# Optimization experiments

Hardware: AMD Instinct MI355X
Metric: run time of the kernel (lower is better)

The kernel has to match this reference:

```python
import jax, jax.numpy as jnp
import numpy as np

B, HF, WF = 16, 32, 32
DIM, NH = 1024, 16
HD = DIM // NH  # 64


def axial_freqs(H, W, head_dim):
    # RotaryEmbedding(dim=head_dim//4, freqs_for='pixel', max_freq=H*W)
    d = head_dim // 4  # rotary dim per axis
    base = jnp.linspace(1.0, (H * W) / 2.0, d // 2) * jnp.pi  # [d//2]
    posH = jnp.linspace(-1.0, 1.0, H)
    posW = jnp.linspace(-1.0, 1.0, W)
    fH = jnp.repeat(posH[:, None] * base[None, :], 2, axis=-1)  # [H, d]
    fW = jnp.repeat(posW[:, None] * base[None, :], 2, axis=-1)  # [W, d]
    fH = jnp.broadcast_to(fH[:, None, :], (H, W, d))
    fW = jnp.broadcast_to(fW[None, :, :], (H, W, d))
    return jnp.concatenate([fH, fW], axis=-1)  # [H, W, 2d] = [H, W, head_dim//2]


def rotate_half(x):
    # interleaved pair rotation: (x1, x2) -> (-x2, x1)
    xr = x.reshape(*x.shape[:-1], -1, 2)
    x1, x2 = xr[..., 0], xr[..., 1]
    return jnp.stack([-x2, x1], axis=-1).reshape(x.shape)


def apply_rotary(freqs, t):
    # t: [B, h, H, W, hd]; freqs: [H, W, rot_dim]
    rd = freqs.shape[-1]
    t_rot, t_pass = t[..., :rd], t[..., rd:]
    t_rot = t_rot * jnp.cos(freqs) + rotate_half(t_rot) * jnp.sin(freqs)
    return jnp.concatenate([t_rot, t_pass], axis=-1)


def setup_inputs() -> dict:
    key = jax.random.key(0)
    k1, k2, k3 = jax.random.split(key, 3)
    s = 1.0 / np.sqrt(DIM)
    return {
        "x": jax.random.normal(k1, (B, HF * WF, DIM), jnp.float32),
        "w_qkv": jax.random.normal(k2, (3 * DIM, DIM), jnp.float32) * s,
        "w_proj": jax.random.normal(k3, (DIM, DIM), jnp.float32) * s,
        "b_proj": jnp.zeros((DIM,), jnp.float32),
    }


def reference(x, w_qkv, w_proj, b_proj):
    freqs = axial_freqs(HF, WF, HD)
    qkv = x @ w_qkv.T  # [B, N, 3*DIM]
    q, k, v = jnp.split(qkv, 3, axis=-1)

    def to_grid(t):  # [B, N, DIM] -> [B, h, H, W, hd]
        return t.reshape(B, HF, WF, NH, HD).transpose(0, 3, 1, 2, 4)

    q, k, v = to_grid(q), to_grid(k), to_grid(v)
    q = apply_rotary(freqs, q)
    k = apply_rotary(freqs, k)
    N = HF * WF
    q = q.reshape(B, NH, N, HD)
    k = k.reshape(B, NH, N, HD)
    v = v.reshape(B, NH, N, HD)

    scale = 1.0 / np.sqrt(HD)
    attn = jax.nn.softmax(jnp.einsum('bhnd,bhmd->bhnm', q, k) * scale, axis=-1)
    out = jnp.einsum('bhnm,bhmd->bhnd', attn, v)  # [B, h, N, hd]
    out = out.transpose(0, 2, 1, 3).reshape(B, N, DIM)
    return out @ w_proj.T + b_proj
```

## Files before the change

### kernel.cpp

```cpp
#include <hip/hip_runtime.h>
#include <hip/hip_bf16.h>
#include <math.h>

typedef __bf16 bf16;
typedef bf16 bf16x4 __attribute__((ext_vector_type(4)));
typedef bf16 bf16x8 __attribute__((ext_vector_type(8)));
typedef float f32x4 __attribute__((ext_vector_type(4)));

#define MFMA16(a, b, c) __builtin_amdgcn_mfma_f32_16x16x32_bf16((a), (b), (c), 0, 0, 0)

#define QSCALE 0.18033688011112042f

__device__ __forceinline__ void async16(const void* g, void* l) {
  __builtin_amdgcn_global_load_lds(
      (const __attribute__((address_space(1))) void*)g,
      (__attribute__((address_space(3))) void*)l, 16, 0, 0);
}

__global__ __launch_bounds__(256) void f2b_kernel(const float* __restrict__ in,
                                                  bf16* __restrict__ out, int n) {
  int i = (blockIdx.x * 256 + threadIdx.x) * 4;
  if (i >= n) return;
  f32x4 v = *(const f32x4*)(in + i);
  bf16x4 o = {(bf16)v[0], (bf16)v[1], (bf16)v[2], (bf16)v[3]};
  *(bf16x4*)(out + i) = o;
}

__global__ __launch_bounds__(256) void table_kernel(float* __restrict__ cosT,
                                                    float* __restrict__ sinT) {
  int idx = blockIdx.x * 256 + threadIdx.x;
  if (idx >= 1024 * 32) return;
  int n = idx >> 5, d = idx & 31;
  int hf = n >> 5, wf = n & 31;
  int bi = (d & 15) >> 1;
  float base = (1.0f + 73.0f * bi) * 3.14159265358979323846f;
  int p = (d < 16) ? hf : wf;
  float pos = (2.0f * (float)p - 31.0f) * (1.0f / 31.0f);
  float f = pos * base;
  cosT[idx] = cosf(f);
  sinT[idx] = sinf(f);
}

template <int EPI, int NBN>
__global__ __launch_bounds__(512, 2) void gemm_bt(
    const bf16* __restrict__ A, const bf16* __restrict__ W,
    bf16* __restrict__ oq, bf16* __restrict__ okk, bf16* __restrict__ ovt,
    const float* __restrict__ cosT, const float* __restrict__ sinT,
    float* __restrict__ outF, const float* __restrict__ bias) {
  constexpr int K = 1024;
  __shared__ bf16 As[4][256 * 32];
  __shared__ bf16 Bs[4][256 * 32];

  const int tid = threadIdx.x;
  const int lane = tid & 63;
  const int wid = tid >> 6;
  const int lo = lane & 15, hi = lane >> 4;
  const int wm = wid >> 2;
  const int wn = wid & 3;

  const int wg = blockIdx.x;
  const int xcd = wg & 7;
  const int i = wg >> 3;
  const int bm = xcd * 8 + i / NBN;
  const int bn = i % NBN;

  const bf16* Ab = A + (size_t)bm * 256 * K;
  const bf16* Wb = W + (size_t)bn * 256 * K;

  const f32x4 fzero = {0.f, 0.f, 0.f, 0.f};
  f32x4 acc[8][4];
#pragma unroll
  for (int i2 = 0; i2 < 8; ++i2)
#pragma unroll
    for (int j = 0; j < 4; ++j) acc[i2][j] = fzero;

  size_t srcOff[2];
  int ldsOff[2];
#pragma unroll
  for (int i2 = 0; i2 < 2; ++i2) {
    const int c = i2 * 512 + tid;
    const int row = c >> 2, g = c & 3;
    const int gsrc = g ^ ((row >> 1) & 3);
    srcOff[i2] = (size_t)row * K + gsrc * 8;
    ldsOff[i2] = c * 8;
  }

  auto stageSlot = [&](int slot, int kh) {
#pragma unroll
    for (int i2 = 0; i2 < 2; ++i2)
      async16(Ab + srcOff[i2] + kh * 32, &As[slot][ldsOff[i2]]);
#pragma unroll
    for (int i2 = 0; i2 < 2; ++i2)
      async16(Wb + srcOff[i2] + kh * 32, &Bs[slot][ldsOff[i2]]);
  };

  auto compute = [&](int slot) {
    bf16x8 af[8], bf[4];
#pragma unroll
    for (int mf = 0; mf < 8; ++mf) {
      const int row = wm * 128 + mf * 16 + lo;
      const int g = hi ^ ((row >> 1) & 3);
      af[mf] = *(const bf16x8*)&As[slot][row * 32 + g * 8];
    }
#pragma unroll
    for (int nf = 0; nf < 4; ++nf) {
      const int row = wn * 64 + nf * 16 + lo;
      const int g = hi ^ ((row >> 1) & 3);
      bf[nf] = *(const bf16x8*)&Bs[slot][row * 32 + g * 8];
    }
    __builtin_amdgcn_s_setprio(1);
#pragma unroll
    for (int mf = 0; mf < 8; ++mf)
#pragma unroll
      for (int nf = 0; nf < 4; ++nf)
        acc[mf][nf] = MFMA16(af[mf], bf[nf], acc[mf][nf]);
    __builtin_amdgcn_s_setprio(0);
  };

  stageSlot(0, 0);
  stageSlot(1, 1);

  for (int kt = 0; kt < 7; ++kt) {
#pragma unroll
    for (int ph = 0; ph < 4; ++ph) {
      stageSlot((ph + 2) & 3, kt * 4 + ph + 2);
      asm volatile("s_waitcnt vmcnt(8)" ::: "memory");
      __builtin_amdgcn_s_barrier();
      compute(ph);
    }
  }
  stageSlot(2, 30);
  asm volatile("s_waitcnt vmcnt(8)" ::: "memory");
  __builtin_amdgcn_s_barrier();
  compute(0);
  stageSlot(3, 31);
  asm volatile("s_waitcnt vmcnt(8)" ::: "memory");
  __builtin_amdgcn_s_barrier();
  compute(1);
  asm volatile("s_waitcnt vmcnt(4)" ::: "memory");
  __builtin_amdgcn_s_barrier();
  compute(2);
  asm volatile("s_waitcnt vmcnt(0)" ::: "memory");
  __builtin_amdgcn_s_barrier();
  compute(3);

  const int rb0 = bm * 256 + wm * 128;
  const int jb0 = bn * 256 + wn * 64;

  if constexpr (EPI == 0) {
#pragma unroll
    for (int ac = 0; ac < 4; ++ac) {
      const int j = jb0 + ac * 16 + lo;
      const int which = j >> 10;
      const int f = j & 1023;
      const int h = f >> 6, d = f & 63;
#pragma unroll
      for (int ar = 0; ar < 8; ++ar) {
        const int rb = rb0 + ar * 16 + 4 * hi;
        f32x4 v = acc[ar][ac];
        if (which == 2) {
          const int b = rb >> 10, n0 = rb & 1023;
          bf16x4 pk = {(bf16)v[0], (bf16)v[1], (bf16)v[2], (bf16)v[3]};
          *(bf16x4*)(ovt + ((size_t)((b * 16 + h) * 64 + d)) * 1024 + n0) = pk;
        } else {
          bf16* dst = which ? okk : oq;
          const float sc = which ? 1.0f : QSCALE;
#pragma unroll
          for (int reg = 0; reg < 4; ++reg) {
            const int r = rb + reg;
            const int b = r >> 10, n = r & 1023;
            float val = v[reg];
            float res;
            if (d < 32) {
              float c = cosT[n * 32 + d];
              float s = sinT[n * 32 + d];
              float pp = __shfl_xor(val, 1);
              res = (d & 1) ? fmaf(val, c, pp * s) : fmaf(val, c, -(pp * s));
            } else {
              res = val;
            }
            dst[((size_t)((b * 16 + h) * 1024 + n)) * 64 + d] = (bf16)(res * sc);
          }
        }
      }
    }
  } else {
#pragma unroll
    for (int ac = 0; ac < 4; ++ac) {
      const int j = jb0 + ac * 16 + lo;
      const float bv = bias[j];
#pragma unroll
      for (int ar = 0; ar < 8; ++ar) {
        const int rb = rb0 + ar * 16 + 4 * hi;
#pragma unroll
        for (int reg = 0; reg < 4; ++reg)
          outF[(size_t)(rb + reg) * 1024 + j] = acc[ar][ac][reg] + bv;
      }
    }
  }
}

__global__ __launch_bounds__(512) void attn_fwd(const bf16* __restrict__ q,
                                                const bf16* __restrict__ k,
                                                const bf16* __restrict__ vt,
                                                bf16* __restrict__ o) {
  constexpr int LDK = 72;
  __shared__ bf16 Kt[2][64 * LDK];
  __shared__ bf16 Vt[2][64 * LDK];
  __shared__ bf16 Pt[8][16 * LDK];
  const int tid = threadIdx.x;
  const int lane = tid & 63, wid = tid >> 6;
  const int lo = lane & 15, hi = lane >> 4;
  const int j = blockIdx.x;
  const int bh = (j & 7) + ((j >> 6) << 3);
  const int qt = (j >> 3) & 7;
  const bf16* qg = q + (size_t)bh * 65536;
  const bf16* kg = k + (size_t)bh * 65536;
  const bf16* vg = vt + (size_t)bh * 65536;

  const int qrow = qt * 128 + wid * 16 + lo;
  const bf16x8 qf0 = *(const bf16x8*)(qg + (size_t)qrow * 64 + 8 * hi);
  const bf16x8 qf1 = *(const bf16x8*)(qg + (size_t)qrow * 64 + 8 * hi + 32);

  const f32x4 fzero = {0.f, 0.f, 0.f, 0.f};
  f32x4 of[4];
  float psum[4] = {0.f, 0.f, 0.f, 0.f};
#pragma unroll
  for (int i = 0; i < 4; ++i) of[i] = fzero;

  const int srow = tid >> 3;
  const int sc0 = (tid & 7) * 8;

  auto stageKV = [&](int buf, int kv) {
    *(bf16x8*)&Kt[buf][srow * LDK + sc0] =
        *(const bf16x8*)(kg + (size_t)(kv * 64 + srow) * 64 + sc0);
    *(bf16x8*)&Vt[buf][srow * LDK + sc0] =
        *(const bf16x8*)(vg + (size_t)srow * 1024 + kv * 64 + sc0);
  };

  stageKV(0, 0);
  __syncthreads();

  for (int kv = 0; kv < 16; ++kv) {
    const int cur = kv & 1;
    if (kv < 15) stageKV(cur ^ 1, kv + 1);

    f32x4 sf[4];
#pragma unroll
    for (int kf = 0; kf < 4; ++kf) {
      bf16x8 kb0 = *(const bf16x8*)&Kt[cur][(kf * 16 + lo) * LDK + 8 * hi];
      bf16x8 kb1 = *(const bf16x8*)&Kt[cur][(kf * 16 + lo) * LDK + 8 * hi + 32];
      f32x4 z = fzero;
      z = MFMA16(qf0, kb0, z);
      z = MFMA16(qf1, kb1, z);
      sf[kf] = z;
    }

#pragma unroll
    for (int kf = 0; kf < 4; ++kf) {
#pragma unroll
      for (int reg = 0; reg < 4; ++reg) {
        float p = __builtin_amdgcn_exp2f(sf[kf][reg]);
        psum[reg] += p;
        Pt[wid][(4 * hi + reg) * LDK + kf * 16 + lo] = (bf16)p;
      }
    }

    const bf16x8 pa0 = *(const bf16x8*)&Pt[wid][lo * LDK + 8 * hi];
    const bf16x8 pa1 = *(const bf16x8*)&Pt[wid][lo * LDK + 8 * hi + 32];
#pragma unroll
    for (int df = 0; df < 4; ++df) {
      bf16x8 vb0 = *(const bf16x8*)&Vt[cur][(df * 16 + lo) * LDK + 8 * hi];
      bf16x8 vb1 = *(const bf16x8*)&Vt[cur][(df * 16 + lo) * LDK + 8 * hi + 32];
      of[df] = MFMA16(pa0, vb0, of[df]);
      of[df] = MFMA16(pa1, vb1, of[df]);
    }
    __syncthreads();
  }

#pragma unroll
  for (int off = 1; off < 16; off <<= 1) {
#pragma unroll
    for (int reg = 0; reg < 4; ++reg) psum[reg] += __shfl_xor(psum[reg], off);
  }

  const int b = bh >> 4, h = bh & 15;
#pragma unroll
  for (int reg = 0; reg < 4; ++reg) {
    const int n = qt * 128 + wid * 16 + 4 * hi + reg;
    const float inv = 1.0f / psum[reg];
#pragma unroll
    for (int df = 0; df < 4; ++df)
      o[((size_t)(b * 1024 + n)) * 1024 + h * 64 + df * 16 + lo] =
          (bf16)(of[df][reg] * inv);
  }
}

extern "C" void kernel_launch(void* const* d_in, const int* in_sizes, int n_in,
                              void* d_out, int out_size, void* d_ws, size_t ws_size,
                              hipStream_t stream) {
  (void)in_sizes; (void)n_in; (void)out_size; (void)ws_size;
  const float* x = (const float*)d_in[0];
  const float* wqkv = (const float*)d_in[1];
  const float* wproj = (const float*)d_in[2];
  const float* bproj = (const float*)d_in[3];

  char* ws = (char*)d_ws;
  bf16* xb = (bf16*)(ws);
  bf16* wqb = (bf16*)(ws + 33554432);
  bf16* wpb = (bf16*)(ws + 39845888);
  float* cosT = (float*)(ws + 41943040);
  float* sinT = (float*)(ws + 42074112);
  bf16* qb = (bf16*)(ws + 42205184);
  bf16* kb = (bf16*)(ws + 75759616);
  bf16* vtb = (bf16*)(ws + 109314048);

  f2b_kernel<<<16384, 256, 0, stream>>>(x, xb, 16 * 1024 * 1024);
  f2b_kernel<<<3072, 256, 0, stream>>>(wqkv, wqb, 3 * 1024 * 1024);
  f2b_kernel<<<1024, 256, 0, stream>>>(wproj, wpb, 1024 * 1024);
  table_kernel<<<128, 256, 0, stream>>>(cosT, sinT);

  gemm_bt<0, 12><<<768, 512, 0, stream>>>(xb, wqb, qb, kb, vtb, cosT, sinT,
                                          nullptr, nullptr);
  attn_fwd<<<2048, 512, 0, stream>>>(qb, kb, vtb, xb);
  gemm_bt<1, 4><<<256, 512, 0, stream>>>(xb, wpb, nullptr, nullptr, nullptr,
                                         nullptr, nullptr, (float*)d_out, bproj);
}
```

Baseline: 302.3 us.

## Double attention query rows per wave with async swizzled K/V staging

Each wave now handles 32 query rows instead of 16, so every K/V fragment read from LDS feeds two row groups of MFMAs. The block count is halved to match. K/V tiles are staged with global_load_lds async copies into an XOR-swizzled unpadded layout, with explicit vmcnt waits, replacing register round-trip stores. The aim is to cut LDS traffic and staging overhead per unit of work, at the cost of more registers and fewer blocks, which may lower occupancy.

After: 285.9 us. 5.4% less time.

```diff
diff --git a/kernel.cpp b/kernel.cpp
--- a/kernel.cpp
+++ b/kernel.cpp
@@ -200,80 +200,104 @@
   }
 }
 
-__global__ __launch_bounds__(512) void attn_fwd(const bf16* __restrict__ q,
-                                                const bf16* __restrict__ k,
-                                                const bf16* __restrict__ vt,
-                                                bf16* __restrict__ o) {
-  constexpr int LDK = 72;
-  __shared__ bf16 Kt[2][64 * LDK];
-  __shared__ bf16 Vt[2][64 * LDK];
-  __shared__ bf16 Pt[8][16 * LDK];
+__global__ __launch_bounds__(512, 4) void attn_fwd(const bf16* __restrict__ q,
+                                                   const bf16* __restrict__ k,
+                                                   const bf16* __restrict__ vt,
+                                                   bf16* __restrict__ o) {
+  __shared__ bf16 Kt[2][64 * 64];
+  __shared__ bf16 Vt[2][64 * 64];
+  __shared__ bf16 Pt[8][32 * 68];
   const int tid = threadIdx.x;
   const int lane = tid & 63, wid = tid >> 6;
   const int lo = lane & 15, hi = lane >> 4;
   const int j = blockIdx.x;
-  const int bh = (j & 7) + ((j >> 6) << 3);
-  const int qt = (j >> 3) & 7;
+  const int bh = (j & 7) + ((j >> 5) << 3);
+  const int qt = (j >> 3) & 3;
   const bf16* qg = q + (size_t)bh * 65536;
   const bf16* kg = k + (size_t)bh * 65536;
   const bf16* vg = vt + (size_t)bh * 65536;
 
-  const int qrow = qt * 128 + wid * 16 + lo;
-  const bf16x8 qf0 = *(const bf16x8*)(qg + (size_t)qrow * 64 + 8 * hi);
-  const bf16x8 qf1 = *(const bf16x8*)(qg + (size_t)qrow * 64 + 8 * hi + 32);
+  bf16x8 qf[2][2];
+#pragma unroll
+  for (int rg = 0; rg < 2; ++rg) {
+    const int qrow = qt * 256 + wid * 32 + rg * 16 + lo;
+#pragma unroll
+    for (int ch = 0; ch < 2; ++ch)
+      qf[rg][ch] = *(const bf16x8*)(qg + (size_t)qrow * 64 + ch * 32 + 8 * hi);
+  }
+
+  const int srow = tid >> 3;
+  const int sgsrc = (tid & 7) ^ (srow & 7);
+  auto stageKV = [&](int buf, int kv) {
+    async16(kg + (size_t)(kv * 64 + srow) * 64 + sgsrc * 8, &Kt[buf][tid * 8]);
+    async16(vg + (size_t)srow * 1024 + kv * 64 + sgsrc * 8, &Vt[buf][tid * 8]);
+  };
+
+  asm volatile("s_waitcnt vmcnt(0)" ::: "memory");
+  stageKV(0, 0);
 
   const f32x4 fzero = {0.f, 0.f, 0.f, 0.f};
-  f32x4 of[4];
-  float psum[4] = {0.f, 0.f, 0.f, 0.f};
-#pragma unroll
-  for (int i = 0; i < 4; ++i) of[i] = fzero;
-
-  const int srow = tid >> 3;
-  const int sc0 = (tid & 7) * 8;
-
-  auto stageKV = [&](int buf, int kv) {
-    *(bf16x8*)&Kt[buf][srow * LDK + sc0] =
-        *(const bf16x8*)(kg + (size_t)(kv * 64 + srow) * 64 + sc0);
-    *(bf16x8*)&Vt[buf][srow * LDK + sc0] =
-        *(const bf16x8*)(vg + (size_t)srow * 1024 + kv * 64 + sc0);
-  };
-
-  stageKV(0, 0);
-  __syncthreads();
+  f32x4 of[2][4];
+  float psum[2][4];
+#pragma unroll
+  for (int rg = 0; rg < 2; ++rg)
+#pragma unroll
+    for (int i = 0; i < 4; ++i) {
+      of[rg][i] = fzero;
+      psum[rg][i >> 2 * 0] = 0.f;
+    }
+#pragma unroll
+  for (int rg = 0; rg < 2; ++rg)
+#pragma unroll
+    for (int r = 0; r < 4; ++r) psum[rg][r] = 0.f;
+
+  const int m7 = lo & 7;
 
   for (int kv = 0; kv < 16; ++kv) {
     const int cur = kv & 1;
-    if (kv < 15) stageKV(cur ^ 1, kv + 1);
-
-    f32x4 sf[4];
+    if (kv < 15) {
+      stageKV(cur ^ 1, kv + 1);
+      asm volatile("s_waitcnt vmcnt(2)" ::: "memory");
+    } else {
+      asm volatile("s_waitcnt vmcnt(0)" ::: "memory");
+    }
+    __builtin_amdgcn_s_barrier();
+
 #pragma unroll
     for (int kf = 0; kf < 4; ++kf) {
-      bf16x8 kb0 = *(const bf16x8*)&Kt[cur][(kf * 16 + lo) * LDK + 8 * hi];
-      bf16x8 kb1 = *(const bf16x8*)&Kt[cur][(kf * 16 + lo) * LDK + 8 * hi + 32];
-      f32x4 z = fzero;
-      z = MFMA16(qf0, kb0, z);
-      z = MFMA16(qf1, kb1, z);
-      sf[kf] = z;
-    }
-
-#pragma unroll
-    for (int kf = 0; kf < 4; ++kf) {
-#pragma unroll
-      for (int reg = 0; reg < 4; ++reg) {
-        float p = __builtin_amdgcn_exp2f(sf[kf][reg]);
-        psum[reg] += p;
-        Pt[wid][(4 * hi + reg) * LDK + kf * 16 + lo] = (bf16)p;
+      const int r = kf * 16 + lo;
+      bf16x8 kb0 = *(const bf16x8*)&Kt[cur][r * 64 + ((hi ^ m7) * 8)];
+      bf16x8 kb1 = *(const bf16x8*)&Kt[cur][r * 64 + (((hi + 4) ^ m7) * 8)];
+#pragma unroll
+      for (int rg = 0; rg < 2; ++rg) {
+        f32x4 z = fzero;
+        z = MFMA16(qf[rg][0], kb0, z);
+        z = MFMA16(qf[rg][1], kb1, z);
+#pragma unroll
+        for (int reg = 0; reg < 4; ++reg) {
+          float p = __builtin_amdgcn_exp2f(z[reg]);
+          psum[rg][reg] += p;
+          Pt[wid][(rg * 16 + 4 * hi + reg) * 68 + kf * 16 + lo] = (bf16)p;
+        }
       }
     }
 
-    const bf16x8 pa0 = *(const bf16x8*)&Pt[wid][lo * LDK + 8 * hi];
-    const bf16x8 pa1 = *(const bf16x8*)&Pt[wid][lo * LDK + 8 * hi + 32];
+    bf16x8 pa[2][2];
+#pragma unroll
+    for (int rg = 0; rg < 2; ++rg)
+#pragma unroll
+      for (int ch = 0; ch < 2; ++ch)
+        pa[rg][ch] = *(const bf16x8*)&Pt[wid][(rg * 16 + lo) * 68 + ch * 32 + 8 * hi];
 #pragma unroll
     for (int df = 0; df < 4; ++df) {
-      bf16x8 vb0 = *(const bf16x8*)&Vt[cur][(df * 16 + lo) * LDK + 8 * hi];
-      bf16x8 vb1 = *(const bf16x8*)&Vt[cur][(df * 16 + lo) * LDK + 8 * hi + 32];
-      of[df] = MFMA16(pa0, vb0, of[df]);
-      of[df] = MFMA16(pa1, vb1, of[df]);
+      const int r = df * 16 + lo;
+      bf16x8 vb0 = *(const bf16x8*)&Vt[cur][r * 64 + ((hi ^ m7) * 8)];
+      bf16x8 vb1 = *(const bf16x8*)&Vt[cur][r * 64 + (((hi + 4) ^ m7) * 8)];
+#pragma unroll
+      for (int rg = 0; rg < 2; ++rg) {
+        of[rg][df] = MFMA16(pa[rg][0], vb0, of[rg][df]);
+        of[rg][df] = MFMA16(pa[rg][1], vb1, of[rg][df]);
+      }
     }
     __syncthreads();
   }
@@ -281,19 +305,23 @@
 #pragma unroll
   for (int off = 1; off < 16; off <<= 1) {
 #pragma unroll
-    for (int reg = 0; reg < 4; ++reg) psum[reg] += __shfl_xor(psum[reg], off);
+    for (int rg = 0; rg < 2; ++rg)
+#pragma unroll
+      for (int reg = 0; reg < 4; ++reg) psum[rg][reg] += __shfl_xor(psum[rg][reg], off);
   }
 
   const int b = bh >> 4, h = bh & 15;
 #pragma unroll
-  for (int reg = 0; reg < 4; ++reg) {
-    const int n = qt * 128 + wid * 16 + 4 * hi + reg;
-    const float inv = 1.0f / psum[reg];
-#pragma unroll
-    for (int df = 0; df < 4; ++df)
-      o[((size_t)(b * 1024 + n)) * 1024 + h * 64 + df * 16 + lo] =
-          (bf16)(of[df][reg] * inv);
-  }
+  for (int rg = 0; rg < 2; ++rg)
+#pragma unroll
+    for (int reg = 0; reg < 4; ++reg) {
+      const int n = qt * 256 + wid * 32 + rg * 16 + 4 * hi + reg;
+      const float inv = 1.0f / psum[rg][reg];
+#pragma unroll
+      for (int df = 0; df < 4; ++df)
+        o[((size_t)(b * 1024 + n)) * 1024 + h * 64 + df * 16 + lo] =
+            (bf16)(of[rg][df][reg] * inv);
+    }
 }
 
 extern "C" void kernel_launch(void* const* d_in, const int* in_sizes, int n_in,
@@ -322,7 +350,7 @@
 
   gemm_bt<0, 12><<<768, 512, 0, stream>>>(xb, wqb, qb, kb, vtb, cosT, sinT,
                                           nullptr, nullptr);
-  attn_fwd<<<2048, 512, 0, stream>>>(qb, kb, vtb, xb);
+  attn_fwd<<<1024, 512, 0, stream>>>(qb, kb, vtb, xb);
   gemm_bt<1, 4><<<256, 512, 0, stream>>>(xb, wpb, nullptr, nullptr, nullptr,
                                          nullptr, nullptr, (float*)d_out, bproj);
 }
```
